# Kernel tuning notes

Measured on AMD Instinct MI355X. Metric: run time of the kernel, lower is better.

The kernel has to match this reference:

```python
import jax, jax.numpy as jnp
import numpy as np

IMG = 800.0
OUT = 7          # output_size
SR = 2           # sampling_ratio
SCALES = (0.25, 0.125, 0.0625, 0.03125)  # FPN strides 4,8,16,32
CANON_SCALE = 224.0
CANON_LVL = 4.0
K_MIN, K_MAX = 2.0, 5.0  # -log2(scales[0]), -log2(scales[-1])
EPS = 1e-6


def setup_inputs() -> dict:
    key = jax.random.key(0)
    k0, k1, k2, k3, kp = jax.random.split(key, 5)
    feat0 = jax.random.normal(k0, (2, 256, 200, 200), dtype=jnp.float32)
    feat1 = jax.random.normal(k1, (2, 256, 100, 100), dtype=jnp.float32)
    feat2 = jax.random.normal(k2, (2, 256, 50, 50), dtype=jnp.float32)
    feat3 = jax.random.normal(k3, (2, 256, 25, 25), dtype=jnp.float32)
    # two random corner points per box, sorted so x0<=x1, y0<=y1
    pts = jax.random.uniform(kp, (2, 512, 2, 2), dtype=jnp.float32) * IMG
    proposals = jnp.concatenate([pts.min(axis=2), pts.max(axis=2)], axis=-1)  # [B,N,4] = x0,y0,x1,y1
    return {"feat0": feat0, "feat1": feat1, "feat2": feat2, "feat3": feat3,
            "proposals": proposals}


def _roi_align(feat, bidx, boxes, scale):
    """torchvision roi_align (aligned=False) for all boxes on one feature map.
    feat: [B,C,H,W], bidx: [N] int32 image index, boxes: [N,4] image coords.
    Returns [N,C,OUT,OUT]."""
    H, W = feat.shape[2], feat.shape[3]
    x0 = boxes[:, 0] * scale
    y0 = boxes[:, 1] * scale
    x1 = boxes[:, 2] * scale
    y1 = boxes[:, 3] * scale
    roi_w = jnp.maximum(x1 - x0, 1.0)
    roi_h = jnp.maximum(y1 - y0, 1.0)
    bin_w = roi_w / OUT
    bin_h = roi_h / OUT
    # sample offsets within the roi, in bin units: [OUT*SR]
    off = (jnp.arange(OUT, dtype=jnp.float32)[:, None]
           + (jnp.arange(SR, dtype=jnp.float32)[None, :] + 0.5) / SR).reshape(-1)
    ys = y0[:, None] + off[None, :] * bin_h[:, None]  # [N, OUT*SR]
    xs = x0[:, None] + off[None, :] * bin_w[:, None]  # [N, OUT*SR]

    def prep(c, size):
        valid = (c >= -1.0) & (c <= float(size))
        cc = jnp.maximum(c, 0.0)
        lo0 = jnp.floor(cc).astype(jnp.int32)
        at_edge = lo0 >= size - 1
        lo = jnp.where(at_edge, size - 1, lo0)
        hi = jnp.where(at_edge, size - 1, lo0 + 1)
        frac = jnp.where(at_edge, 0.0, cc - lo0.astype(cc.dtype))
        return lo, hi, frac, valid

    yl, yh, ly, vy = prep(ys, H)
    xl, xh, lx, vx = prep(xs, W)
    hy, hx = 1.0 - ly, 1.0 - lx
    b3 = bidx[:, None, None]

    def gather(yi, xi):
        # advanced indices (b, y, x) with channel slice -> [N, Sy, Sx, C]
        return feat[b3, :, yi[:, :, None], xi[:, None, :]]

    val = ((hy[:, :, None] * hx[:, None, :])[..., None] * gather(yl, xl)
           + (hy[:, :, None] * lx[:, None, :])[..., None] * gather(yl, xh)
           + (ly[:, :, None] * hx[:, None, :])[..., None] * gather(yh, xl)
           + (ly[:, :, None] * lx[:, None, :])[..., None] * gather(yh, xh))
    mask = (vy[:, :, None] & vx[:, None, :]).astype(val.dtype)[..., None]
    val = val * mask
    N, C = boxes.shape[0], feat.shape[1]
    val = val.reshape(N, OUT, SR, OUT, SR, C).mean(axis=(2, 4))  # avg over samples
    return val.transpose(0, 3, 1, 2)  # [N, C, OUT, OUT]


def reference(feat0, feat1, feat2, feat3, proposals):
    feats = (feat0, feat1, feat2, feat3)
    B, Np = proposals.shape[0], proposals.shape[1]
    boxes = proposals.reshape(-1, 4)                      # [N,4]
    bidx = jnp.repeat(jnp.arange(B, dtype=jnp.int32), Np)  # image id per roi
    # LevelMapper: FPN paper heuristic
    areas = (boxes[:, 2] - boxes[:, 0]) * (boxes[:, 3] - boxes[:, 1])
    s = jnp.sqrt(areas)
    lvls = jnp.floor(CANON_LVL + jnp.log2(s / CANON_SCALE + EPS))
    lvls = (jnp.clip(lvls, K_MIN, K_MAX) - K_MIN).astype(jnp.int32)  # 0..3
    N, C = boxes.shape[0], feat0.shape[1]
    result = jnp.zeros((N, C, OUT, OUT), dtype=feat0.dtype)
    for l, (feat, scale) in enumerate(zip(feats, SCALES)):
        pooled = _roi_align(feat, bidx, boxes, scale)
        result = result + jnp.where((lvls == l)[:, None, None, None], pooled, 0.0)
    return result
```

## Files before the change

kernel.cpp:

```cpp
#include <hip/hip_runtime.h>
#include <hip/hip_fp16.h>
#include <math.h>

#define POUT 7
#define NCH 256

typedef float v4f __attribute__((ext_vector_type(4)));

#define HW0 40000
#define HW1 10000
#define HW2 2500
#define HW3 625
#define WS_OFF0 0
#define WS_OFF1 (2*NCH*HW0)
#define WS_OFF2 (WS_OFF1 + 2*NCH*HW1)
#define WS_OFF3 (WS_OFF2 + 2*NCH*HW2)
#define WS_ELEMS (WS_OFF3 + 2*NCH*HW3)
#define WS_SLACK 512
#define WS_PERM_BYTE ((size_t)(WS_ELEMS + WS_SLACK) * 2)
#define WS_NEED (WS_PERM_BYTE + 1024 * sizeof(int))

#define TP 56
#define RS 114
#define NT0 ((HW0 + TP - 1) / TP)
#define NT1 ((HW1 + TP - 1) / TP)
#define NT2 ((HW2 + TP - 1) / TP)
#define NT3 ((HW3 + TP - 1) / TP)
#define NBLK ((NT0 + NT1 + NT2 + NT3) * 4)

__global__ __launch_bounds__(512, 8) void transpose_fused_kernel(
    const float* __restrict__ f0, const float* __restrict__ f1,
    const float* __restrict__ f2, const float* __restrict__ f3,
    __half* __restrict__ ws, const float* __restrict__ props,
    int boxes_per_img, int N)
{
    __shared__ float tile[64 * RS];

    const int gid = blockIdx.x;
    int id = gid;
    const float* src; int HW, nt; size_t woff;
    if (id < NT0 * 4)                        { src = f0; HW = HW0; nt = NT0; woff = WS_OFF0; }
    else if ((id -= NT0 * 4) < NT1 * 4)      { src = f1; HW = HW1; nt = NT1; woff = WS_OFF1; }
    else if ((id -= NT1 * 4) < NT2 * 4)      { src = f2; HW = HW2; nt = NT2; woff = WS_OFF2; }
    else { id -= NT2 * 4;                      src = f3; HW = HW3; nt = NT3; woff = WS_OFF3; }

    const int ch = id & 1;
    const int tl = (id >> 1) % nt;
    const int bb = (id >> 1) / nt;
    const int p0 = tl * TP;
    const int pn = min(TP, HW - p0);
    const int c0 = ch * 128;
    const int t  = threadIdx.x;

    const float* sbase = src + ((size_t)(bb * NCH + c0)) * HW + p0;

    if (pn == TP) {
        for (int i = t; i < 128 * (TP / 4); i += 512) {
            const int c  = i / (TP / 4);
            const int p4 = i - c * (TP / 4);
            const v4f v = __builtin_nontemporal_load(
                (const v4f*)&sbase[(size_t)c * HW + p4 * 4]);
            float* d = &tile[(c >> 1) * RS + (c & 1) + p4 * 8];
            d[0] = v[0]; d[2] = v[1]; d[4] = v[2]; d[6] = v[3];
        }
    } else {
        for (int i = t; i < 128 * (TP / 4); i += 512) {
            const int c  = i / (TP / 4);
            const int pb = (i - c * (TP / 4)) * 4;
            float vv[4];
            #pragma unroll
            for (int k = 0; k < 4; ++k)
                vv[k] = (pb + k < pn) ? sbase[(size_t)c * HW + pb + k] : 0.0f;
            float* d = &tile[(c >> 1) * RS + (c & 1) + pb * 2];
            d[0] = vv[0]; d[2] = vv[1]; d[4] = vv[2]; d[6] = vv[3];
        }
    }
    __syncthreads();

    __half* dbase = ws + woff + ((size_t)bb * HW + p0) * NCH + c0;
    for (int i = t; i < 64 * TP; i += 512) {
        const int c2 = i & 63, p = i >> 6;
        if (p < pn) {
            const float2 v = *(const float2*)&tile[c2 * RS + 2 * p];
            *(__half2*)&dbase[(size_t)p * NCH + 2 * c2] = __floats2half2_rn(v.x, v.y);
        }
    }

    if (gid == 0) {
        __syncthreads();
        unsigned* keys = (unsigned*)tile;
        if (N == 1024) {
            for (int i = t; i < 1024; i += 512) {
                const float4 box = ((const float4*)props)[i];
                const float area = (box.z - box.x) * (box.w - box.y);
                float lvlf = floorf(4.0f + log2f(sqrtf(area) / 224.0f + 1e-6f));
                lvlf = fminf(fmaxf(lvlf, 2.0f), 5.0f) - 2.0f;
                const int l = (int)lvlf;
                const float sc = 0.25f / (float)(1 << l);
                int yc = (int)(0.5f * (box.y + box.w) * sc);
                int xc = (int)(0.5f * (box.x + box.z) * sc);
                yc = yc < 0 ? 0 : (yc > 255 ? 255 : yc);
                xc = xc < 0 ? 0 : (xc > 255 ? 255 : xc);
                const unsigned hi = (unsigned)((i / boxes_per_img) * 4 + l);
                keys[i] = (((hi << 8 | (unsigned)yc) << 8 | (unsigned)xc) << 10) | (unsigned)i;
            }
            for (int size = 2; size <= 1024; size <<= 1)
                for (int stride = size >> 1; stride > 0; stride >>= 1) {
                    __syncthreads();
                    const int lo = t & (stride - 1);
                    const int k  = ((t ^ lo) << 1) | lo;
                    const unsigned a = keys[k], b2 = keys[k + stride];
                    if ((a > b2) == ((k & size) == 0)) { keys[k] = b2; keys[k + stride] = a; }
                }
            __syncthreads();
            int* perm = (int*)((char*)ws + WS_PERM_BYTE);
            for (int i = t; i < 1024; i += 512) {
                const unsigned k = keys[i];
                perm[i] = (int)((k & 1023u) | (((k >> 26) & 3u) << 10) | ((k >> 28) << 12));
            }
        }
        if (t < 256) ((unsigned*)(ws + WS_ELEMS))[t] = 0u;
    }
}

__global__ __launch_bounds__(256, 4) void roi_gather_kernel(
    const __half* __restrict__ ws, const float* __restrict__ props,
    float* __restrict__ out, int boxes_per_img)
{
    __shared__ int2   sOff[196];
    __shared__ float4 sW[196];
    __shared__ __align__(16) float sStage[64 * 49];

    const int* perm = (const int*)((const char*)ws + WS_PERM_BYTE);
    const int pe = perm[(blockIdx.x & 7) * 128 + (blockIdx.x >> 3)];
    const int n = pe & 1023;
    const int l = (pe >> 10) & 3;
    const int b = pe >> 12;
    const int t = threadIdx.x;

    int sz; size_t lvl_off;
    if      (l == 0) { sz = 200; lvl_off = WS_OFF0; }
    else if (l == 1) { sz = 100; lvl_off = WS_OFF1; }
    else if (l == 2) { sz = 50;  lvl_off = WS_OFF2; }
    else             { sz = 25;  lvl_off = WS_OFF3; }
    const int HW = sz * sz;
    const float scale = 0.25f / (float)(1 << l);

    if (t < 196) {
        const float4 box = ((const float4*)props)[n];
        const int bin = t >> 2, sub = t & 3;
        const int ph = bin / POUT, pw = bin % POUT;
        const int iy = sub >> 1,  ix = sub & 1;

        const float x0 = box.x * scale, y0 = box.y * scale;
        const float x1 = box.z * scale, y1 = box.w * scale;
        const float bin_w = fmaxf(x1 - x0, 1.0f) / (float)POUT;
        const float bin_h = fmaxf(y1 - y0, 1.0f) / (float)POUT;

        const float ys = y0 + ((float)ph + ((float)iy + 0.5f) * 0.5f) * bin_h;
        const float xs = x0 + ((float)pw + ((float)ix + 0.5f) * 0.5f) * bin_w;

        const bool  vy  = (ys >= -1.0f) && (ys <= (float)sz);
        const float cy  = fmaxf(ys, 0.0f);
        const int   yl0 = (int)floorf(cy);
        const bool  ey  = yl0 >= sz - 1;
        const int   yl  = ey ? sz - 1 : yl0;
        const int   yh  = ey ? sz - 1 : yl0 + 1;
        const float ly  = ey ? 0.0f : cy - (float)yl0;

        const bool  vx  = (xs >= -1.0f) && (xs <= (float)sz);
        const float cx  = fmaxf(xs, 0.0f);
        const int   xl0 = (int)floorf(cx);
        const bool  ex  = xl0 >= sz - 1;
        const int   xl  = ex ? sz - 1 : xl0;
        const float lx  = ex ? 0.0f : cx - (float)xl0;

        const float hy = 1.0f - ly, hx = 1.0f - lx;
        const float m  = (vy && vx) ? 0.25f : 0.0f;
        sOff[t] = make_int2((yl * sz + xl) * NCH, (yh * sz + xl) * NCH);
        sW[t]   = make_float4(hy * hx * m, hy * lx * m, ly * hx * m, ly * lx * m);
    }
    __syncthreads();

    const int c2 = t & 127;
    const int hf = t >> 7;
    const int bin0 = hf * 24;
    const __half* fb = ws + lvl_off + (size_t)b * (size_t)HW * NCH + 2 * c2;

    float2 acc[25];
    #pragma unroll
    for (int j = 0; j < 25; ++j) { acc[j].x = 0.0f; acc[j].y = 0.0f; }

    #pragma unroll
    for (int j = 0; j < 25; ++j) {
        const int rbase = (bin0 + j) * 4;
        #pragma unroll
        for (int s = 0; s < 4; ++s) {
            const int2   o = sOff[rbase + s];
            const float4 w = sW[rbase + s];
            const float2 v00 = __half22float2(*(const __half2*)&fb[o.x]);
            const float2 v01 = __half22float2(*(const __half2*)&fb[o.x + NCH]);
            const float2 v10 = __half22float2(*(const __half2*)&fb[o.y]);
            const float2 v11 = __half22float2(*(const __half2*)&fb[o.y + NCH]);
            acc[j].x += w.x * v00.x + w.y * v01.x + w.z * v10.x + w.w * v11.x;
            acc[j].y += w.x * v00.y + w.y * v01.y + w.z * v10.y + w.w * v11.y;
        }
    }

    __syncthreads();
    float* obase = out + (size_t)n * (NCH * 49);
    #pragma unroll
    for (int r = 0; r < 4; ++r) {
        if ((c2 >> 5) == r) {
            const int lc = (c2 & 31) * 2;
            if (hf == 0) {
                #pragma unroll
                for (int j = 0; j < 25; ++j) {
                    sStage[lc * 49 + j]       = acc[j].x;
                    sStage[(lc + 1) * 49 + j] = acc[j].y;
                }
            } else {
                #pragma unroll
                for (int j = 1; j < 25; ++j) {
                    sStage[lc * 49 + 24 + j]       = acc[j].x;
                    sStage[(lc + 1) * 49 + 24 + j] = acc[j].y;
                }
            }
        }
        __syncthreads();
        v4f* d4 = (v4f*)(obase + r * (64 * 49));
        const v4f* s4 = (const v4f*)sStage;
        for (int i = t; i < 64 * 49 / 4; i += 256)
            __builtin_nontemporal_store(s4[i], &d4[i]);
        __syncthreads();
    }
}

__global__ __launch_bounds__(256, 4) void roi_align_nchw_kernel(
    const float* __restrict__ f0, const float* __restrict__ f1,
    const float* __restrict__ f2, const float* __restrict__ f3,
    const float* __restrict__ props, float* __restrict__ out, int boxes_per_img)
{
    const int n = blockIdx.x;
    const int t = threadIdx.x;
    if (t >= 196) return;
    const int bin = t >> 2, q = t & 3;
    const int ph = bin / POUT, pw = bin % POUT;
    const int iy = q >> 1,    ix = q & 1;
    const int b = n / boxes_per_img;

    const float4 box = ((const float4*)props)[n];
    const float area = (box.z - box.x) * (box.w - box.y);
    float lvlf = floorf(4.0f + log2f(sqrtf(area) / 224.0f + 1e-6f));
    lvlf = fminf(fmaxf(lvlf, 2.0f), 5.0f) - 2.0f;
    const int l = (int)lvlf;

    const float* feat; int sz;
    if      (l == 0) { feat = f0; sz = 200; }
    else if (l == 1) { feat = f1; sz = 100; }
    else if (l == 2) { feat = f2; sz = 50;  }
    else             { feat = f3; sz = 25;  }
    const float scale = 0.25f / (float)(1 << l);

    const float x0 = box.x * scale, y0 = box.y * scale;
    const float x1 = box.z * scale, y1 = box.w * scale;
    const float bin_w = fmaxf(x1 - x0, 1.0f) / (float)POUT;
    const float bin_h = fmaxf(y1 - y0, 1.0f) / (float)POUT;
    const float ysamp = y0 + ((float)ph + ((float)iy + 0.5f) * 0.5f) * bin_h;
    const float xsamp = x0 + ((float)pw + ((float)ix + 0.5f) * 0.5f) * bin_w;

    const bool  vy  = (ysamp >= -1.0f) && (ysamp <= (float)sz);
    const float cy  = fmaxf(ysamp, 0.0f);
    const int   yl0 = (int)floorf(cy);
    const bool  ey  = yl0 >= sz - 1;
    const int   yl  = ey ? sz - 1 : yl0;
    const int   yh  = ey ? sz - 1 : yl0 + 1;
    const float ly  = ey ? 0.0f : cy - (float)yl0;
    const bool  vx  = (xsamp >= -1.0f) && (xsamp <= (float)sz);
    const float cx  = fmaxf(xsamp, 0.0f);
    const int   xl0 = (int)floorf(cx);
    const bool  ex  = xl0 >= sz - 1;
    const int   xl  = ex ? sz - 1 : xl0;
    const int   xh  = ex ? sz - 1 : xl0 + 1;
    const float lx  = ex ? 0.0f : cx - (float)xl0;

    const float hy = 1.0f - ly, hx = 1.0f - lx;
    const float m  = (vy && vx) ? 1.0f : 0.0f;
    const float w00 = hy * hx * m, w01 = hy * lx * m;
    const float w10 = ly * hx * m, w11 = ly * lx * m;

    const int HW = sz * sz;
    const float* base = feat + (size_t)b * NCH * HW;
    int o00 = yl * sz + xl, o01 = yl * sz + xh;
    int o10 = yh * sz + xl, o11 = yh * sz + xh;
    float* op = out + (size_t)n * NCH * (POUT * POUT) + bin;

    #pragma unroll 4
    for (int cch = 0; cch < NCH; ++cch) {
        float v = w00 * base[o00] + w01 * base[o01]
                + w10 * base[o10] + w11 * base[o11];
        v += __shfl_xor(v, 1);
        v += __shfl_xor(v, 2);
        if (q == 0) op[cch * (POUT * POUT)] = v * 0.25f;
        o00 += HW; o01 += HW; o10 += HW; o11 += HW;
    }
}

extern "C" void kernel_launch(void* const* d_in, const int* in_sizes, int n_in,
                              void* d_out, int out_size, void* d_ws, size_t ws_size,
                              hipStream_t stream) {
    const float* f0 = (const float*)d_in[0];
    const float* f1 = (const float*)d_in[1];
    const float* f2 = (const float*)d_in[2];
    const float* f3 = (const float*)d_in[3];
    const float* props = (const float*)d_in[4];
    float* out = (float*)d_out;

    const int N = in_sizes[4] / 4;
    const int B = in_sizes[0] / (NCH * HW0);
    const int boxes_per_img = N / B;

    if (ws_size >= WS_NEED && B == 2 && N == 1024) {
        __half* wsh = (__half*)d_ws;
        transpose_fused_kernel<<<NBLK, 512, 0, stream>>>(f0, f1, f2, f3, wsh,
                                                         props, boxes_per_img, N);
        roi_gather_kernel<<<N, 256, 0, stream>>>(wsh, props, out, boxes_per_img);
    } else {
        roi_align_nchw_kernel<<<N, 256, 0, stream>>>(f0, f1, f2, f3, props, out, boxes_per_img);
    }
}
```

Before: 192.0 us.

## Widen ROI gather to 4 channels per thread and split bins four ways

The pooling kernel now has each thread handle 4 fp16 channels through 8-byte loads and split the 49 bins into four groups of 13/12, instead of 2 channels with a 25-bin half split. This halves the number of gather load instructions, so each corner fetch covers more bytes per lane. The transpose pass writes 4 halves per store, and the fp32 read uses a plain float4 load instead of a nontemporal one. The cost is a dynamic-index loop when writing accumulators to shared memory, which may push acc into scratch memory, and a duplicated clamped bin 48 in the last group.

```diff
diff --git a/kernel.cpp b/kernel.cpp
--- a/kernel.cpp
+++ b/kernel.cpp
@@ -58,10 +58,9 @@
         for (int i = t; i < 128 * (TP / 4); i += 512) {
             const int c  = i / (TP / 4);
             const int p4 = i - c * (TP / 4);
-            const v4f v = __builtin_nontemporal_load(
-                (const v4f*)&sbase[(size_t)c * HW + p4 * 4]);
+            const float4 v = *(const float4*)&sbase[(size_t)c * HW + p4 * 4];
             float* d = &tile[(c >> 1) * RS + (c & 1) + p4 * 8];
-            d[0] = v[0]; d[2] = v[1]; d[4] = v[2]; d[6] = v[3];
+            d[0] = v.x; d[2] = v.y; d[4] = v.z; d[6] = v.w;
         }
     } else {
         for (int i = t; i < 128 * (TP / 4); i += 512) {
@@ -78,11 +77,17 @@
     __syncthreads();
 
     __half* dbase = ws + woff + ((size_t)bb * HW + p0) * NCH + c0;
-    for (int i = t; i < 64 * TP; i += 512) {
-        const int c2 = i & 63, p = i >> 6;
+    for (int i = t; i < 32 * TP; i += 512) {
+        const int u2 = i & 31, p = i >> 5;
         if (p < pn) {
-            const float2 v = *(const float2*)&tile[c2 * RS + 2 * p];
-            *(__half2*)&dbase[(size_t)p * NCH + 2 * c2] = __floats2half2_rn(v.x, v.y);
+            const float2 a = *(const float2*)&tile[(2 * u2    ) * RS + 2 * p];
+            const float2 c2v = *(const float2*)&tile[(2 * u2 + 1) * RS + 2 * p];
+            const __half2 h0 = __floats2half2_rn(a.x, a.y);
+            const __half2 h1 = __floats2half2_rn(c2v.x, c2v.y);
+            uint2 w;
+            w.x = *reinterpret_cast<const unsigned*>(&h0);
+            w.y = *reinterpret_cast<const unsigned*>(&h1);
+            *(uint2*)&dbase[(size_t)p * NCH + 4 * u2] = w;
         }
     }
 
@@ -182,28 +187,41 @@
     }
     __syncthreads();
 
-    const int c2 = t & 127;
-    const int hf = t >> 7;
-    const int bin0 = hf * 24;
-    const __half* fb = ws + lvl_off + (size_t)b * (size_t)HW * NCH + 2 * c2;
-
-    float2 acc[25];
+    const int c4 = t & 63;
+    const int qt = t >> 6;
+    const int bstart = (qt == 0) ? 0 : 13 + 12 * (qt - 1);
+    const int bcnt   = (qt == 0) ? 13 : 12;
+    const __half* fb = ws + lvl_off + (size_t)b * (size_t)HW * NCH + 4 * c4;
+
+    float acc[13][4];
     #pragma unroll
-    for (int j = 0; j < 25; ++j) { acc[j].x = 0.0f; acc[j].y = 0.0f; }
+    for (int j = 0; j < 13; ++j)
+        #pragma unroll
+        for (int k = 0; k < 4; ++k) acc[j][k] = 0.0f;
 
     #pragma unroll
-    for (int j = 0; j < 25; ++j) {
-        const int rbase = (bin0 + j) * 4;
+    for (int j = 0; j < 13; ++j) {
+        const int bin = min(bstart + j, 48);
         #pragma unroll
         for (int s = 0; s < 4; ++s) {
-            const int2   o = sOff[rbase + s];
-            const float4 w = sW[rbase + s];
-            const float2 v00 = __half22float2(*(const __half2*)&fb[o.x]);
-            const float2 v01 = __half22float2(*(const __half2*)&fb[o.x + NCH]);
-            const float2 v10 = __half22float2(*(const __half2*)&fb[o.y]);
-            const float2 v11 = __half22float2(*(const __half2*)&fb[o.y + NCH]);
-            acc[j].x += w.x * v00.x + w.y * v01.x + w.z * v10.x + w.w * v11.x;
-            acc[j].y += w.x * v00.y + w.y * v01.y + w.z * v10.y + w.w * v11.y;
+            const int2   o = sOff[bin * 4 + s];
+            const float4 w = sW[bin * 4 + s];
+            const uint2 r00 = *(const uint2*)&fb[o.x];
+            const uint2 r01 = *(const uint2*)&fb[o.x + NCH];
+            const uint2 r10 = *(const uint2*)&fb[o.y];
+            const uint2 r11 = *(const uint2*)&fb[o.y + NCH];
+            const float2 a00 = __half22float2(*(const __half2*)&r00.x);
+            const float2 b00 = __half22float2(*(const __half2*)&r00.y);
+            const float2 a01 = __half22float2(*(const __half2*)&r01.x);
+            const float2 b01 = __half22float2(*(const __half2*)&r01.y);
+            const float2 a10 = __half22float2(*(const __half2*)&r10.x);
+            const float2 b10 = __half22float2(*(const __half2*)&r10.y);
+            const float2 a11 = __half22float2(*(const __half2*)&r11.x);
+            const float2 b11 = __half22float2(*(const __half2*)&r11.y);
+            acc[j][0] += w.x * a00.x + w.y * a01.x + w.z * a10.x + w.w * a11.x;
+            acc[j][1] += w.x * a00.y + w.y * a01.y + w.z * a10.y + w.w * a11.y;
+            acc[j][2] += w.x * b00.x + w.y * b01.x + w.z * b10.x + w.w * b11.x;
+            acc[j][3] += w.x * b00.y + w.y * b01.y + w.z * b10.y + w.w * b11.y;
         }
     }
 
@@ -211,21 +229,12 @@
     float* obase = out + (size_t)n * (NCH * 49);
     #pragma unroll
     for (int r = 0; r < 4; ++r) {
-        if ((c2 >> 5) == r) {
-            const int lc = (c2 & 31) * 2;
-            if (hf == 0) {
+        if ((c4 >> 4) == r) {
+            const int lc = (c4 & 15) * 4;
+            for (int j = 0; j < bcnt; ++j)
                 #pragma unroll
-                for (int j = 0; j < 25; ++j) {
-                    sStage[lc * 49 + j]       = acc[j].x;
-                    sStage[(lc + 1) * 49 + j] = acc[j].y;
-                }
-            } else {
-                #pragma unroll
-                for (int j = 1; j < 25; ++j) {
-                    sStage[lc * 49 + 24 + j]       = acc[j].x;
-                    sStage[(lc + 1) * 49 + 24 + j] = acc[j].y;
-                }
-            }
+                for (int k = 0; k < 4; ++k)
+                    sStage[(lc + k) * 49 + bstart + j] = acc[j][k];
         }
         __syncthreads();
         v4f* d4 = (v4f*)(obase + r * (64 * 49));
```

Result: slower. 228.4 us (+18.9%).
